# Kernel tuning notes

Hardware: AMD Instinct MI355X
Metric: run time of the kernel (lower is better)

Reference implementation:

```python
import jax, jax.numpy as jnp
import numpy as np

B, DIM, N = 8, 512, 1024
EMB, CDIM, M = 128, 512, 256
HEADS, DHEAD = 8, 64
DFF = 4 * DIM  # GEGLU inner dim


def _group_norm(x, g, b, groups=32, eps=1e-6):
    # x: [B, C, L]
    Bx, C, L = x.shape
    xr = x.reshape(Bx, groups, (C // groups) * L)
    mu = xr.mean(-1, keepdims=True)
    var = xr.var(-1, keepdims=True)
    xn = ((xr - mu) * jax.lax.rsqrt(var + eps)).reshape(Bx, C, L)
    return xn * g[None, :, None] + b[None, :, None]


def _layer_norm(x, g, b, eps=1e-5):
    mu = x.mean(-1, keepdims=True)
    var = x.var(-1, keepdims=True)
    return (x - mu) * jax.lax.rsqrt(var + eps) * g + b


def _attention(x, ctx, wq, wk, wv, wo, bo, heads):
    # x: [B, Nq, Dq], ctx: [B, Nk, Dk]
    Bx, Nq, _ = x.shape
    q = x @ wq.T
    k = ctx @ wk.T
    v = ctx @ wv.T
    d = q.shape[-1] // heads
    sp = lambda t: t.reshape(Bx, -1, heads, d).transpose(0, 2, 1, 3)  # b h n d
    q, k, v = sp(q), sp(k), sp(v)
    sim = jnp.einsum('bhid,bhjd->bhij', q, k) * (d ** -0.5)
    o = jnp.einsum('bhij,bhjd->bhid', jax.nn.softmax(sim, axis=-1), v)
    o = o.transpose(0, 2, 1, 3).reshape(Bx, Nq, heads * d)
    return o @ wo.T + bo


def setup_inputs() -> dict:
    key = jax.random.key(0)
    ks = jax.random.split(key, 16)
    rn = lambda k, sh: jax.random.normal(k, sh, dtype=jnp.float32) * 0.02
    inner = HEADS * DHEAD
    z = lambda n: jnp.zeros((n,), jnp.float32)
    o = lambda n: jnp.ones((n,), jnp.float32)
    return {
        'x': jax.random.normal(ks[0], (B, DIM, N), dtype=jnp.float32),
        'emb': jax.random.normal(ks[1], (B, EMB), dtype=jnp.float32),
        'context': jax.random.normal(ks[2], (B, CDIM, M), dtype=jnp.float32),
        'w_emb': rn(ks[3], (2 * DIM, EMB)), 'b_emb': z(2 * DIM),
        'gn_g': o(DIM), 'gn_b': z(DIM),
        'conv_w': rn(ks[4], (DIM, DIM)), 'conv_b': z(DIM),
        'a1_wq': rn(ks[5], (inner, DIM)), 'a1_wk': rn(ks[6], (inner, DIM)),
        'a1_wv': rn(ks[7], (inner, DIM)), 'a1_wo': rn(ks[8], (DIM, inner)), 'a1_bo': z(DIM),
        'a2_wq': rn(ks[9], (inner, DIM)), 'a2_wk': rn(ks[10], (inner, CDIM)),
        'a2_wv': rn(ks[11], (inner, CDIM)), 'a2_wo': rn(ks[12], (DIM, inner)), 'a2_bo': z(DIM),
        'ln1_g': o(DIM), 'ln1_b': z(DIM),
        'ln2_g': o(DIM), 'ln2_b': z(DIM),
        'ln3_g': o(DIM), 'ln3_b': z(DIM),
        'ff_w1': rn(ks[13], (2 * DFF, DIM)), 'ff_b1': z(2 * DFF),
        'ff_w2': rn(ks[14], (DIM, DFF)), 'ff_b2': z(DIM),
    }


def reference(x, emb, context, w_emb, b_emb, gn_g, gn_b, conv_w, conv_b,
              a1_wq, a1_wk, a1_wv, a1_wo, a1_bo,
              a2_wq, a2_wk, a2_wv, a2_wo, a2_bo,
              ln1_g, ln1_b, ln2_g, ln2_b, ln3_g, ln3_b,
              ff_w1, ff_b1, ff_w2, ff_b2):
    # scale-shift modulated GroupNorm + SiLU + 1x1 Conv1d residual branch
    emb_out = (jax.nn.silu(emb) @ w_emb.T + b_emb)[:, :, None]  # [B, 2*dim, 1]
    scale, shift = jnp.split(emb_out, 2, axis=1)
    h = _group_norm(x, gn_g, gn_b) * (1.0 + scale) + shift
    h = jnp.einsum('oc,bcn->bon', conv_w, jax.nn.silu(h)) + conv_b[None, :, None]
    x = x + h
    # to token-major layout
    xt = x.transpose(0, 2, 1)          # [B, N, dim]
    ctx = context.transpose(0, 2, 1)   # [B, M, context_dim]
    # self attention
    y = _layer_norm(xt, ln1_g, ln1_b)
    xt = _attention(y, y, a1_wq, a1_wk, a1_wv, a1_wo, a1_bo, HEADS) + xt
    # cross attention
    xt = _attention(_layer_norm(xt, ln2_g, ln2_b), ctx,
                    a2_wq, a2_wk, a2_wv, a2_wo, a2_bo, HEADS) + xt
    # GEGLU feed-forward
    u = _layer_norm(xt, ln3_g, ln3_b) @ ff_w1.T + ff_b1
    a, g = jnp.split(u, 2, axis=-1)
    xt = (a * jax.nn.gelu(g, approximate=False)) @ ff_w2.T + ff_b2 + xt
    return xt.transpose(0, 2, 1)  # back to [B, dim, N]
```

## Files before the change

kernel.cpp:

```cpp
#include <hip/hip_runtime.h>
#include <math.h>

#define NB 8
#define CDIM 512
#define NT 1024
#define MT 256
#define DFFI 2048

typedef short bf16x8 __attribute__((ext_vector_type(8)));
typedef float f32x4 __attribute__((ext_vector_type(4)));

__device__ __forceinline__ float sigmoidf_(float v){ return 1.0f/(1.0f+__expf(-v)); }

__device__ __forceinline__ short f2bf(float f){
    union { float f; unsigned u; } v; v.f = f;
    unsigned r = v.u + 0x7FFFu + ((v.u >> 16) & 1u);
    return (short)(r >> 16);
}

#define GLDS(gp, lp) __builtin_amdgcn_global_load_lds( \
    (const __attribute__((address_space(1))) void*)(gp), \
    (__attribute__((address_space(3))) void*)(lp), 16, 0, 0)

__global__ void cvt_all(const float* __restrict__ a1wq, const float* __restrict__ a1wk,
                        const float* __restrict__ a1wv, const float* __restrict__ a1wo,
                        const float* __restrict__ a2wq, const float* __restrict__ a2wk,
                        const float* __restrict__ a2wv, const float* __restrict__ a2wo,
                        const float* __restrict__ ffw1, const float* __restrict__ ffw2,
                        const float* __restrict__ convw, short* __restrict__ WB){
    int e = (blockIdx.x*256 + threadIdx.x)*8;
    if (e >= 5505024) return;
    const float* src; int off;
    if (e < 2097152){
        const float* tbl[8] = {a1wq,a1wk,a1wv,a1wo,a2wq,a2wk,a2wv,a2wo};
        src = tbl[e >> 18]; off = e & 262143;
    } else if (e < 4194304){ src = ffw1; off = e - 2097152; }
    else if (e < 5242880){ src = ffw2; off = e - 4194304; }
    else { src = convw; off = e - 5242880; }
    float4 x0 = ((const float4*)(src+off))[0], x1 = ((const float4*)(src+off))[1];
    bf16x8 v;
    v[0]=f2bf(x0.x); v[1]=f2bf(x0.y); v[2]=f2bf(x0.z); v[3]=f2bf(x0.w);
    v[4]=f2bf(x1.x); v[5]=f2bf(x1.y); v[6]=f2bf(x1.z); v[7]=f2bf(x1.w);
    *(bf16x8*)(WB + e) = v;
}


__global__ void emb_gemm(const float* __restrict__ emb, const float* __restrict__ w,
                         const float* __restrict__ bias, float* __restrict__ out){
    int idx = blockIdx.x*256 + threadIdx.x;
    int b = idx >> 10, o = idx & 1023;
    const float* e = emb + b*128;
    const float* wr = w + (size_t)o*128;
    float acc = 0.f;
    for (int i=0;i<128;i++){ float ev=e[i]; acc += (ev*sigmoidf_(ev))*wr[i]; }
    out[idx] = acc + bias[o];
}

__global__ void gn_stats(const float* __restrict__ x, float* __restrict__ stats){
    int bg = blockIdx.x;
    const float* base = x + (size_t)bg*16*NT;
    float s=0.f, sq=0.f;
    for (int i=threadIdx.x; i<16*NT; i+=256){ float v = base[i]; s+=v; sq+=v*v; }
    __shared__ float rs[256], rq[256];
    rs[threadIdx.x]=s; rq[threadIdx.x]=sq; __syncthreads();
    for (int st=128; st>0; st>>=1){
        if (threadIdx.x<st){ rs[threadIdx.x]+=rs[threadIdx.x+st]; rq[threadIdx.x]+=rq[threadIdx.x+st]; }
        __syncthreads();
    }
    if (threadIdx.x==0){
        float mu = rs[0]/(16.f*NT);
        float var = rq[0]/(16.f*NT) - mu*mu;
        stats[2*bg] = mu; stats[2*bg+1] = rsqrtf(var + 1e-6f);
    }
}

__global__ void mod_act(const float* __restrict__ x, const float* __restrict__ stats,
                        const float* __restrict__ gg, const float* __restrict__ gb,
                        const float* __restrict__ ss, short* __restrict__ act_t){
    __shared__ float tile[32][33];
    int n0 = blockIdx.x*32, c0 = blockIdx.y*32, b = blockIdx.z;
    int tx = threadIdx.x, ty = threadIdx.y;
    #pragma unroll
    for (int k=0;k<4;k++){
        int c = c0 + ty + k*8;
        tile[ty+k*8][tx] = x[((size_t)(b*CDIM+c))*NT + n0 + tx];
    }
    __syncthreads();
    #pragma unroll
    for (int k=0;k<4;k++){
        int c = c0 + tx, n = n0 + ty + k*8;
        float raw = tile[tx][ty+k*8];
        int gi = b*32 + (c>>4);
        float v = (raw - stats[2*gi]) * stats[2*gi+1] * gg[c] + gb[c];
        v = v * (1.f + ss[b*1024 + c]) + ss[b*1024 + 512 + c];
        act_t[((size_t)(b*NT+n))*CDIM + c] = f2bf(v * sigmoidf_(v));
    }
}

__global__ void ln_rows(const float* __restrict__ in, const float* __restrict__ g,
                        const float* __restrict__ bta, short* __restrict__ out){
    int row = blockIdx.x;
    const float* base = in + (size_t)row*CDIM;
    int t = threadIdx.x;
    float v0 = base[t], v1 = base[t+256];
    __shared__ float rs[256], rq[256];
    rs[t]=v0+v1; rq[t]=v0*v0+v1*v1; __syncthreads();
    for (int st=128; st>0; st>>=1){
        if (t<st){ rs[t]+=rs[t+st]; rq[t]+=rq[t+st]; }
        __syncthreads();
    }
    float mu = rs[0]*(1.f/512.f);
    float var = rq[0]*(1.f/512.f) - mu*mu;
    float rstd = rsqrtf(var + 1e-5f);
    out[(size_t)row*CDIM + t]     = f2bf((v0-mu)*rstd*g[t]+bta[t]);
    out[(size_t)row*CDIM + t+256] = f2bf((v1-mu)*rstd*g[t+256]+bta[t+256]);
}

__global__ void transpose_ctx(const float* __restrict__ in, short* __restrict__ out){
    __shared__ float tile[32][33];
    int m0 = blockIdx.x*32, c0 = blockIdx.y*32, b = blockIdx.z;
    int tx=threadIdx.x, ty=threadIdx.y;
    #pragma unroll
    for (int k=0;k<4;k++){
        int c = c0+ty+k*8;
        tile[ty+k*8][tx] = in[((size_t)(b*512+c))*MT + m0+tx];
    }
    __syncthreads();
    #pragma unroll
    for (int k=0;k<4;k++){
        int m = m0+ty+k*8, c = c0+tx;
        out[((size_t)(b*MT+m))*512 + c] = f2bf(tile[tx][ty+k*8]);
    }
}

__global__ void transpose_out(const float* __restrict__ in, float* __restrict__ out){
    __shared__ float tile[32][33];
    int n0 = blockIdx.x*32, c0 = blockIdx.y*32, b=blockIdx.z;
    int tx=threadIdx.x, ty=threadIdx.y;
    #pragma unroll
    for (int k=0;k<4;k++){
        int n = n0+ty+k*8;
        tile[ty+k*8][tx] = in[((size_t)(b*NT+n))*512 + c0+tx];
    }
    __syncthreads();
    #pragma unroll
    for (int k=0;k<4;k++){
        int c = c0+ty+k*8, n = n0+tx;
        out[((size_t)(b*512+c))*NT + n] = tile[tx][ty+k*8];
    }
}

__global__ __launch_bounds__(256,2) void gemm_bb(
        const short* __restrict__ A, const short* __restrict__ W,
        const float* __restrict__ bias, const float* __restrict__ res,
        float* __restrict__ outf, short* __restrict__ outb,
        int K, int O, int ostr, int resmode){
    __shared__ short As[128*64];
    __shared__ short Bs[64*64];
    int r0 = blockIdx.x*128, o0 = blockIdx.y*64;
    int tid = threadIdx.x, w = tid>>6, lane = tid&63;
    int quad = lane>>4, lw = lane&15;
    int g_row = lane>>3, g_s = lane&7;
    int sseg = g_s ^ g_row;
    int wr = (w&1)*64, wc = (w>>1)*32;
    f32x4 acc[4][2] = {};
    for (int k0 = 0; k0 < K; k0 += 64){
        #pragma unroll
        for (int j=0;j<4;j++){
            int row = w*32 + j*8 + g_row;
            GLDS(A + (size_t)(r0+row)*K + k0 + sseg*8, As + (w*32+j*8)*64);
        }
        #pragma unroll
        for (int j=0;j<2;j++){
            int row = w*16 + j*8 + g_row;
            GLDS(W + (size_t)(o0+row)*K + k0 + sseg*8, Bs + (w*16+j*8)*64);
        }
        __syncthreads();
        bf16x8 af[4][2], bf[2][2];
        #pragma unroll
        for (int ks=0; ks<2; ks++){
            #pragma unroll
            for (int i=0;i<4;i++){
                int row = wr + i*16 + lw;
                af[i][ks] = *(const bf16x8*)&As[row*64 + (((ks*4+quad) ^ (lw&7)))*8];
            }
            #pragma unroll
            for (int j=0;j<2;j++){
                int col = wc + j*16 + lw;
                bf[j][ks] = *(const bf16x8*)&Bs[col*64 + (((ks*4+quad) ^ (lw&7)))*8];
            }
        }
        #pragma unroll
        for (int ks=0; ks<2; ks++)
            #pragma unroll
            for (int i=0;i<4;i++)
                #pragma unroll
                for (int j=0;j<2;j++)
                    acc[i][j] = __builtin_amdgcn_mfma_f32_16x16x32_bf16(af[i][ks], bf[j][ks], acc[i][j], 0, 0, 0);
        __syncthreads();
    }
    #pragma unroll
    for (int i=0;i<4;i++){
        #pragma unroll
        for (int j=0;j<2;j++){
            #pragma unroll
            for (int reg=0; reg<4; reg++){
                int row = r0 + wr + i*16 + quad*4 + reg;
                int col = o0 + wc + j*16 + lw;
                float v = acc[i][j][reg];
                if (bias) v += bias[col];
                if (resmode==1) v += res[(size_t)row*O + col];
                else if (resmode==2){
                    int b = row >> 10, n = row & 1023;
                    v += res[((size_t)(b*CDIM+col))*NT + n];
                }
                if (outf) outf[(size_t)row*ostr + col] = v;
                else      outb[(size_t)row*ostr + col] = f2bf(v);
            }
        }
    }
}

__global__ __launch_bounds__(256,2) void ff1_geglu_bb(
        const short* __restrict__ A, const short* __restrict__ W,
        const float* __restrict__ b1, short* __restrict__ out){
    __shared__ short As[128*64];
    __shared__ short Ba[64*64];
    __shared__ short Bg[64*64];
    int r0 = blockIdx.x*128, j0 = blockIdx.y*64;
    int tid = threadIdx.x, w = tid>>6, lane = tid&63;
    int quad = lane>>4, lw = lane&15;
    int g_row = lane>>3, g_s = lane&7;
    int sseg = g_s ^ g_row;
    int wr = (w&1)*64, wc = (w>>1)*32;
    f32x4 acca[4][2] = {}, accg[4][2] = {};
    for (int k0 = 0; k0 < 512; k0 += 64){
        #pragma unroll
        for (int j=0;j<4;j++){
            int row = w*32 + j*8 + g_row;
            GLDS(A + (size_t)(r0+row)*512 + k0 + sseg*8, As + (w*32+j*8)*64);
        }
        #pragma unroll
        for (int j=0;j<2;j++){
            int row = w*16 + j*8 + g_row;
            GLDS(W + (size_t)(j0+row)*512 + k0 + sseg*8, Ba + (w*16+j*8)*64);
            GLDS(W + (size_t)(2048+j0+row)*512 + k0 + sseg*8, Bg + (w*16+j*8)*64);
        }
        __syncthreads();
        bf16x8 af[4][2], ba[2][2], bg[2][2];
        #pragma unroll
        for (int ks=0; ks<2; ks++){
            #pragma unroll
            for (int i=0;i<4;i++){
                int row = wr + i*16 + lw;
                af[i][ks] = *(const bf16x8*)&As[row*64 + (((ks*4+quad) ^ (lw&7)))*8];
            }
            #pragma unroll
            for (int j=0;j<2;j++){
                int col = wc + j*16 + lw;
                ba[j][ks] = *(const bf16x8*)&Ba[col*64 + (((ks*4+quad) ^ (lw&7)))*8];
                bg[j][ks] = *(const bf16x8*)&Bg[col*64 + (((ks*4+quad) ^ (lw&7)))*8];
            }
        }
        #pragma unroll
        for (int ks=0; ks<2; ks++)
            #pragma unroll
            for (int i=0;i<4;i++)
                #pragma unroll
                for (int j=0;j<2;j++){
                    acca[i][j] = __builtin_amdgcn_mfma_f32_16x16x32_bf16(af[i][ks], ba[j][ks], acca[i][j], 0, 0, 0);
                    accg[i][j] = __builtin_amdgcn_mfma_f32_16x16x32_bf16(af[i][ks], bg[j][ks], accg[i][j], 0, 0, 0);
                }
        __syncthreads();
    }
    #pragma unroll
    for (int i=0;i<4;i++){
        #pragma unroll
        for (int j=0;j<2;j++){
            #pragma unroll
            for (int reg=0; reg<4; reg++){
                int row = r0 + wr + i*16 + quad*4 + reg;
                int col = j0 + wc + j*16 + lw;
                float a = acca[i][j][reg] + b1[col];
                float g = accg[i][j][reg] + b1[2048+col];
                float gl = 0.5f*g*(1.0f + erff(g*0.70710678118654752f));
                out[(size_t)row*DFFI + col] = f2bf(a*gl);
            }
        }
    }
}

__global__ __launch_bounds__(256) void attn_fa(
        const short* __restrict__ q, const short* __restrict__ k,
        const short* __restrict__ vt, short* __restrict__ o,
        int Nq, int Nk, int qstr, int kstr, int vtstr, float sc_log2e){
    __shared__ short Ks[64*64];
    __shared__ short Vs[64*64];
    __shared__ short QP[64*64];
    int bh = blockIdx.x & 63;
    int qt = blockIdx.x >> 6;
    int b = bh >> 3, h = bh & 7;
    int tid = threadIdx.x, w = tid>>6, lane = tid&63;
    int quad = lane>>4, lw = lane&15;
    int lrow = lane>>3, lg = (lane&7) ^ (lane>>3);
    int q0 = qt*64;

    #pragma unroll
    for (int t=0;t<2;t++){
        int row = w*16 + t*8 + lrow;
        GLDS(q + (size_t)(b*Nq + q0 + row)*qstr + h*64 + lg*8, QP + (w*16+t*8)*64);
    }
    __syncthreads();
    bf16x8 qf[2];
    {
        int r = w*16 + lw;
        qf[0] = *(const bf16x8*)&QP[r*64 + (( quad      ^ (r&7))*8)];
        qf[1] = *(const bf16x8*)&QP[r*64 + (((quad+4) ^ (r&7))*8)];
    }

    f32x4 oacc[4] = {};
    f32x4 accl = {};
    bf16x8 ones;
    #pragma unroll
    for (int i=0;i<8;i++) ones[i] = (short)0x3F80;

    int nkt = Nk >> 6;
    for (int kt = 0; kt < nkt; kt++){
        __syncthreads();
        #pragma unroll
        for (int t=0;t<2;t++){
            int row = w*16 + t*8 + lrow;
            GLDS(k  + (size_t)(b*Nk + kt*64 + row)*kstr + h*64 + lg*8, Ks + (w*16+t*8)*64);
            GLDS(vt + (size_t)(h*64 + row)*vtstr + b*Nk + kt*64 + lg*8, Vs + (w*16+t*8)*64);
        }
        __syncthreads();

        f32x4 s[4] = {};
        #pragma unroll
        for (int ct=0;ct<4;ct++){
            int r = ct*16 + lw;
            bf16x8 kf0 = *(const bf16x8*)&Ks[r*64 + (( quad      ^ (r&7))*8)];
            bf16x8 kf1 = *(const bf16x8*)&Ks[r*64 + (((quad+4) ^ (r&7))*8)];
            s[ct] = __builtin_amdgcn_mfma_f32_16x16x32_bf16(qf[0], kf0, s[ct], 0,0,0);
            s[ct] = __builtin_amdgcn_mfma_f32_16x16x32_bf16(qf[1], kf1, s[ct], 0,0,0);
        }

        #pragma unroll
        for (int ct=0;ct<4;ct++){
            int colb = (((ct+quad)&3)*16) + lw;
            #pragma unroll
            for (int r=0;r<4;r++){
                float p = exp2f(s[ct][r]*sc_log2e);
                union { float f; unsigned u; } uv; uv.f = p;
                QP[(w*16 + quad*4 + r)*64 + colb] = (short)(uv.u >> 16);
            }
        }
        __asm__ volatile("s_waitcnt lgkmcnt(0)" ::: "memory");

        bf16x8 pf[2];
        {
            int r = w*16 + lw;
            int rot = (lw>>2)&3;
            pf[0] = *(const bf16x8*)&QP[r*64 + (((    (quad>>1) + rot)&3)*16) + (quad&1)*8];
            pf[1] = *(const bf16x8*)&QP[r*64 + (((2 + (quad>>1) + rot)&3)*16) + (quad&1)*8];
        }
        accl = __builtin_amdgcn_mfma_f32_16x16x32_bf16(pf[0], ones, accl, 0,0,0);
        accl = __builtin_amdgcn_mfma_f32_16x16x32_bf16(pf[1], ones, accl, 0,0,0);
        #pragma unroll
        for (int dt=0; dt<4; dt++){
            int r = dt*16 + lw;
            bf16x8 vf0 = *(const bf16x8*)&Vs[r*64 + (( quad      ^ (r&7))*8)];
            bf16x8 vf1 = *(const bf16x8*)&Vs[r*64 + (((quad+4) ^ (r&7))*8)];
            oacc[dt] = __builtin_amdgcn_mfma_f32_16x16x32_bf16(pf[0], vf0, oacc[dt], 0,0,0);
            oacc[dt] = __builtin_amdgcn_mfma_f32_16x16x32_bf16(pf[1], vf1, oacc[dt], 0,0,0);
        }
    }
    float inv[4];
    #pragma unroll
    for (int r=0;r<4;r++) inv[r] = 1.0f/accl[r];
    #pragma unroll
    for (int dt=0; dt<4; dt++){
        #pragma unroll
        for (int r=0;r<4;r++){
            int qi = q0 + w*16 + quad*4 + r;
            o[(size_t)(b*Nq + qi)*512 + h*64 + dt*16 + lw] = f2bf(oacc[dt][r]*inv[r]);
        }
    }
}

extern "C" void kernel_launch(void* const* d_in, const int* in_sizes, int n_in,
                              void* d_out, int out_size, void* d_ws, size_t ws_size,
                              hipStream_t stream) {
    const float* x      = (const float*)d_in[0];
    const float* emb    = (const float*)d_in[1];
    const float* context= (const float*)d_in[2];
    const float* w_emb  = (const float*)d_in[3];
    const float* b_emb  = (const float*)d_in[4];
    const float* gn_g   = (const float*)d_in[5];
    const float* gn_b   = (const float*)d_in[6];
    const float* conv_w = (const float*)d_in[7];
    const float* conv_b = (const float*)d_in[8];
    const float* a1_wq  = (const float*)d_in[9];
    const float* a1_wk  = (const float*)d_in[10];
    const float* a1_wv  = (const float*)d_in[11];
    const float* a1_wo  = (const float*)d_in[12];
    const float* a1_bo  = (const float*)d_in[13];
    const float* a2_wq  = (const float*)d_in[14];
    const float* a2_wk  = (const float*)d_in[15];
    const float* a2_wv  = (const float*)d_in[16];
    const float* a2_wo  = (const float*)d_in[17];
    const float* a2_bo  = (const float*)d_in[18];
    const float* ln1_g  = (const float*)d_in[19];
    const float* ln1_b  = (const float*)d_in[20];
    const float* ln2_g  = (const float*)d_in[21];
    const float* ln2_b  = (const float*)d_in[22];
    const float* ln3_g  = (const float*)d_in[23];
    const float* ln3_b  = (const float*)d_in[24];
    const float* ff_w1  = (const float*)d_in[25];
    const float* ff_b1  = (const float*)d_in[26];
    const float* ff_w2  = (const float*)d_in[27];
    const float* ff_b2  = (const float*)d_in[28];
    float* out = (float*)d_out;

    char* base = (char*)d_ws;
    float* SS    = (float*)base;
    float* STATS = SS + 8192;
    float* F0    = (float*)(base + 65536);
    float* F1    = F0 + 4194304;
    short* WB    = (short*)(F1 + 4194304);
    short* qkW   = WB;
    short* vW    = WB + 524288;
    short* wo1W  = WB + 786432;
    short* a2qW  = WB + 1048576;
    short* a2kW  = WB + 1310720;
    short* a2vW  = WB + 1572864;
    short* wo2W  = WB + 1835008;
    short* ffw1W = WB + 2097152;
    short* ffw2W = WB + 4194304;
    short* convW = WB + 5242880;
    short* CTXb  = WB + 5505024;
    short* L0    = CTXb + 1048576;
    short* BIG   = L0 + 4194304;
    short* Q0    = BIG;
    short* VT1   = BIG + 8388608;
    short* AO    = BIG + 12582912;
    short* A2Q   = BIG;
    short* K2    = BIG + 4194304;
    short* VT2   = BIG + 5242880;
    short* ACT2  = BIG;

    dim3 tb(32,8);
    const float SCL2E = 0.125f * 1.4426950408889634f;

    cvt_all<<<2688,256,0,stream>>>(a1_wq,a1_wk,a1_wv,a1_wo,a2_wq,a2_wk,a2_wv,a2_wo,
                                   ff_w1,ff_w2,conv_w, WB);

    emb_gemm<<<32,256,0,stream>>>(emb, w_emb, b_emb, SS);
    gn_stats<<<256,256,0,stream>>>(x, STATS);
    mod_act<<<dim3(32,16,8), tb, 0, stream>>>(x, STATS, gn_g, gn_b, SS, L0);
    transpose_ctx<<<dim3(8,16,8), tb, 0, stream>>>(context, CTXb);
    gemm_bb<<<dim3(64,8),256,0,stream>>>(L0, convW, conv_b, x, F0, nullptr, 512, 512, 512, 2);

    ln_rows<<<8192,256,0,stream>>>(F0, ln1_g, ln1_b, L0);
    gemm_bb<<<dim3(64,16),256,0,stream>>>(L0, qkW, nullptr, nullptr, nullptr, Q0, 512, 1024, 1024, 0);
    gemm_bb<<<dim3(4,128),256,0,stream>>>(vW, L0, nullptr, nullptr, nullptr, VT1, 512, 8192, 8192, 0);
    attn_fa<<<1024,256,0,stream>>>(Q0, Q0+512, VT1, AO, 1024, 1024, 1024, 1024, 8192, SCL2E);
    gemm_bb<<<dim3(64,8),256,0,stream>>>(AO, wo1W, a1_bo, F0, F1, nullptr, 512, 512, 512, 1);

    ln_rows<<<8192,256,0,stream>>>(F1, ln2_g, ln2_b, L0);
    gemm_bb<<<dim3(64,8),256,0,stream>>>(L0, a2qW, nullptr, nullptr, nullptr, A2Q, 512, 512, 512, 0);
    gemm_bb<<<dim3(16,8),256,0,stream>>>(CTXb, a2kW, nullptr, nullptr, nullptr, K2, 512, 512, 512, 0);
    gemm_bb<<<dim3(4,32),256,0,stream>>>(a2vW, CTXb, nullptr, nullptr, nullptr, VT2, 512, 2048, 2048, 0);
    attn_fa<<<1024,256,0,stream>>>(A2Q, K2, VT2, AO, 1024, 256, 512, 512, 2048, SCL2E);
    gemm_bb<<<dim3(64,8),256,0,stream>>>(AO, wo2W, a2_bo, F1, F0, nullptr, 512, 512, 512, 1);

    ln_rows<<<8192,256,0,stream>>>(F0, ln3_g, ln3_b, L0);
    ff1_geglu_bb<<<dim3(64,32),256,0,stream>>>(L0, ffw1W, ff_b1, ACT2);
    gemm_bb<<<dim3(64,8),256,0,stream>>>(ACT2, ffw2W, ff_b2, F0, F1, nullptr, 2048, 512, 512, 1);
    transpose_out<<<dim3(32,16,8), tb, 0, stream>>>(F1, out);
}
```

Measured before the change: 467.0 us.

## Double-buffer GEMM LDS loads and use wave-per-row LayerNorm

The bf16 GEMM now keeps two LDS buffers. It issues the global-to-LDS loads for the next K tile before computing on the current one, and replaces __syncthreads with explicit vmcnt/lgkmcnt waits and barriers. This is meant to hide global load latency behind the MFMA work. LayerNorm is also rewritten so each 64-lane wavefront handles one row with vectorized float4 loads and shuffle reductions, removing the shared-memory tree reduction and its many barriers. The trade-off is double the LDS per block, which may reduce occupancy, and the hand-set vmcnt(6) relies on exactly six outstanding loads per thread.

After: 469.8 us. Within noise of the previous version (+0.6%).

```diff
diff --git a/kernel.cpp b/kernel.cpp
--- a/kernel.cpp
+++ b/kernel.cpp
@@ -99,21 +99,28 @@
 
 __global__ void ln_rows(const float* __restrict__ in, const float* __restrict__ g,
                         const float* __restrict__ bta, short* __restrict__ out){
-    int row = blockIdx.x;
-    const float* base = in + (size_t)row*CDIM;
-    int t = threadIdx.x;
-    float v0 = base[t], v1 = base[t+256];
-    __shared__ float rs[256], rq[256];
-    rs[t]=v0+v1; rq[t]=v0*v0+v1*v1; __syncthreads();
-    for (int st=128; st>0; st>>=1){
-        if (t<st){ rs[t]+=rs[t+st]; rq[t]+=rq[t+st]; }
-        __syncthreads();
-    }
-    float mu = rs[0]*(1.f/512.f);
-    float var = rq[0]*(1.f/512.f) - mu*mu;
-    float rstd = rsqrtf(var + 1e-5f);
-    out[(size_t)row*CDIM + t]     = f2bf((v0-mu)*rstd*g[t]+bta[t]);
-    out[(size_t)row*CDIM + t+256] = f2bf((v1-mu)*rstd*g[t+256]+bta[t+256]);
+    int row = blockIdx.x*4 + (threadIdx.x>>6);
+    int lane = threadIdx.x & 63;
+    const float* base = in + (size_t)row*CDIM + lane*8;
+    float4 a = ((const float4*)base)[0], b4 = ((const float4*)base)[1];
+    float vals[8] = {a.x,a.y,a.z,a.w,b4.x,b4.y,b4.z,b4.w};
+    float s = 0.f, q = 0.f;
+    #pragma unroll
+    for (int i=0;i<8;i++){ s += vals[i]; q += vals[i]*vals[i]; }
+    #pragma unroll
+    for (int off=32; off>0; off>>=1){ s += __shfl_xor(s, off); q += __shfl_xor(q, off); }
+    float mu = s*(1.f/512.f);
+    float rstd = rsqrtf(q*(1.f/512.f) - mu*mu + 1e-5f);
+    const float* gp = g + lane*8;
+    const float* bp = bta + lane*8;
+    float4 g0=((const float4*)gp)[0], g1=((const float4*)gp)[1];
+    float4 e0=((const float4*)bp)[0], e1=((const float4*)bp)[1];
+    float gs[8] = {g0.x,g0.y,g0.z,g0.w,g1.x,g1.y,g1.z,g1.w};
+    float es[8] = {e0.x,e0.y,e0.z,e0.w,e1.x,e1.y,e1.z,e1.w};
+    bf16x8 o8;
+    #pragma unroll
+    for (int i=0;i<8;i++) o8[i] = f2bf((vals[i]-mu)*rstd*gs[i] + es[i]);
+    *(bf16x8*)(out + (size_t)row*CDIM + lane*8) = o8;
 }
 
 __global__ void transpose_ctx(const float* __restrict__ in, short* __restrict__ out){
@@ -155,39 +162,54 @@
         const float* __restrict__ bias, const float* __restrict__ res,
         float* __restrict__ outf, short* __restrict__ outb,
         int K, int O, int ostr, int resmode){
-    __shared__ short As[128*64];
-    __shared__ short Bs[64*64];
+    __shared__ short As[2][128*64];
+    __shared__ short Bs[2][64*64];
     int r0 = blockIdx.x*128, o0 = blockIdx.y*64;
     int tid = threadIdx.x, w = tid>>6, lane = tid&63;
     int quad = lane>>4, lw = lane&15;
     int g_row = lane>>3, g_s = lane&7;
     int sseg = g_s ^ g_row;
     int wr = (w&1)*64, wc = (w>>1)*32;
+    const short* Abase = A + (size_t)r0*K;
+    const short* Wbase = W + (size_t)o0*K;
     f32x4 acc[4][2] = {};
-    for (int k0 = 0; k0 < K; k0 += 64){
+
+    auto issue = [&](int buf, int kk){
         #pragma unroll
         for (int j=0;j<4;j++){
             int row = w*32 + j*8 + g_row;
-            GLDS(A + (size_t)(r0+row)*K + k0 + sseg*8, As + (w*32+j*8)*64);
+            GLDS(Abase + (size_t)row*K + kk + sseg*8, &As[buf][(w*32+j*8)*64]);
         }
         #pragma unroll
         for (int j=0;j<2;j++){
             int row = w*16 + j*8 + g_row;
-            GLDS(W + (size_t)(o0+row)*K + k0 + sseg*8, Bs + (w*16+j*8)*64);
-        }
-        __syncthreads();
+            GLDS(Wbase + (size_t)row*K + kk + sseg*8, &Bs[buf][(w*16+j*8)*64]);
+        }
+    };
+
+    issue(0, 0);
+    int nk = K >> 6;
+    for (int it=0; it<nk; ++it){
+        int cur = it & 1;
+        if (it+1 < nk){
+            issue(cur^1, (it+1)<<6);
+            __asm__ volatile("s_waitcnt vmcnt(6)" ::: "memory");
+        } else {
+            __asm__ volatile("s_waitcnt vmcnt(0)" ::: "memory");
+        }
+        __builtin_amdgcn_s_barrier();
         bf16x8 af[4][2], bf[2][2];
         #pragma unroll
         for (int ks=0; ks<2; ks++){
             #pragma unroll
             for (int i=0;i<4;i++){
                 int row = wr + i*16 + lw;
-                af[i][ks] = *(const bf16x8*)&As[row*64 + (((ks*4+quad) ^ (lw&7)))*8];
+                af[i][ks] = *(const bf16x8*)&As[cur][row*64 + (((ks*4+quad) ^ (lw&7)))*8];
             }
             #pragma unroll
             for (int j=0;j<2;j++){
                 int col = wc + j*16 + lw;
-                bf[j][ks] = *(const bf16x8*)&Bs[col*64 + (((ks*4+quad) ^ (lw&7)))*8];
+                bf[j][ks] = *(const bf16x8*)&Bs[cur][col*64 + (((ks*4+quad) ^ (lw&7)))*8];
             }
         }
         #pragma unroll
@@ -197,7 +219,8 @@
                 #pragma unroll
                 for (int j=0;j<2;j++)
                     acc[i][j] = __builtin_amdgcn_mfma_f32_16x16x32_bf16(af[i][ks], bf[j][ks], acc[i][j], 0, 0, 0);
-        __syncthreads();
+        __asm__ volatile("s_waitcnt lgkmcnt(0)" ::: "memory");
+        __builtin_amdgcn_s_barrier();
     }
     #pragma unroll
     for (int i=0;i<4;i++){
@@ -461,20 +484,20 @@
     transpose_ctx<<<dim3(8,16,8), tb, 0, stream>>>(context, CTXb);
     gemm_bb<<<dim3(64,8),256,0,stream>>>(L0, convW, conv_b, x, F0, nullptr, 512, 512, 512, 2);
 
-    ln_rows<<<8192,256,0,stream>>>(F0, ln1_g, ln1_b, L0);
+    ln_rows<<<2048,256,0,stream>>>(F0, ln1_g, ln1_b, L0);
     gemm_bb<<<dim3(64,16),256,0,stream>>>(L0, qkW, nullptr, nullptr, nullptr, Q0, 512, 1024, 1024, 0);
     gemm_bb<<<dim3(4,128),256,0,stream>>>(vW, L0, nullptr, nullptr, nullptr, VT1, 512, 8192, 8192, 0);
     attn_fa<<<1024,256,0,stream>>>(Q0, Q0+512, VT1, AO, 1024, 1024, 1024, 1024, 8192, SCL2E);
     gemm_bb<<<dim3(64,8),256,0,stream>>>(AO, wo1W, a1_bo, F0, F1, nullptr, 512, 512, 512, 1);
 
-    ln_rows<<<8192,256,0,stream>>>(F1, ln2_g, ln2_b, L0);
+    ln_rows<<<2048,256,0,stream>>>(F1, ln2_g, ln2_b, L0);
     gemm_bb<<<dim3(64,8),256,0,stream>>>(L0, a2qW, nullptr, nullptr, nullptr, A2Q, 512, 512, 512, 0);
     gemm_bb<<<dim3(16,8),256,0,stream>>>(CTXb, a2kW, nullptr, nullptr, nullptr, K2, 512, 512, 512, 0);
     gemm_bb<<<dim3(4,32),256,0,stream>>>(a2vW, CTXb, nullptr, nullptr, nullptr, VT2, 512, 2048, 2048, 0);
     attn_fa<<<1024,256,0,stream>>>(A2Q, K2, VT2, AO, 1024, 256, 512, 512, 2048, SCL2E);
     gemm_bb<<<dim3(64,8),256,0,stream>>>(AO, wo2W, a2_bo, F1, F0, nullptr, 512, 512, 512, 1);
 
-    ln_rows<<<8192,256,0,stream>>>(F0, ln3_g, ln3_b, L0);
+    ln_rows<<<2048,256,0,stream>>>(F0, ln3_g, ln3_b, L0);
     ff1_geglu_bb<<<dim3(64,32),256,0,stream>>>(L0, ffw1W, ff_b1, ACT2);
     gemm_bb<<<dim3(64,8),256,0,stream>>>(ACT2, ffw2W, ff_b2, F0, F1, nullptr, 2048, 512, 512, 1);
     transpose_out<<<dim3(32,16,8), tb, 0, stream>>>(F1, out);
```
